# Performance work log

Hardware: AMD Instinct MI355X
Metric: run time of the kernel (lower is better)

## Reference

```python
import jax, jax.numpy as jnp
import numpy as np

NUM_HEADS = 2
POOL_K = 256
REPEAT = 20


def setup_inputs() -> dict:
    key = jax.random.key(0)
    k1, k2, k3 = jax.random.split(key, 3)
    C = 6144
    d = C // NUM_HEADS                      # 3072
    N = REPEAT * (d // POOL_K)              # 240, required by Pq add
    x = jax.random.normal(k1, (N, C), dtype=jnp.float32)
    w_qkv = jax.random.normal(k2, (3 * C, C), dtype=jnp.float32) * 0.02
    w_proj = jax.random.normal(k3, (C, C), dtype=jnp.float32) * 0.02
    b_proj = jnp.zeros((C,), dtype=jnp.float32)
    return {"x": x, "w_qkv": w_qkv, "w_proj": w_proj, "b_proj": b_proj}


def reference(x, w_qkv, w_proj, b_proj):
    N, C = x.shape
    H = NUM_HEADS
    d = C // H
    scale = d ** -0.5
    # qkv: (N, 3C) -> (N, 3, H, d) -> (3, H, N, d)
    qkv = (x @ w_qkv.T).reshape(N, 3, H, d).transpose(1, 2, 0, 3)
    q, k, v = qkv[0], qkv[1], qkv[2]        # each (H, N, d)
    # MaxPool1d(256) over last dim, then tile x20 along last dim -> (H, N, N)
    Pq = q.reshape(H, N, d // POOL_K, POOL_K).max(axis=-1)
    Pq = jnp.tile(Pq, (1, 1, REPEAT))       # (H, N, N)
    attn = jnp.einsum('hnd,hmd->hnm', q, k) * scale + 0.1 * Pq
    attn = jax.nn.softmax(attn, axis=-1)
    out = jnp.einsum('hnm,hmd->hnd', attn, v)    # (H, N, d)
    out = out.transpose(1, 0, 2).reshape(N, C)
    return out @ w_proj.T + b_proj
```

## Files before the change

### kernel.cpp

```cpp
#include <hip/hip_runtime.h>
#include <hip/hip_bf16.h>

#define NN 240
#define CC 6144
#define DD 3072
#define C3 18432
#define HH 2

typedef __attribute__((ext_vector_type(8))) short bf16x8;
typedef __attribute__((ext_vector_type(4))) float f32x4;
typedef unsigned short ushort_t;

static __device__ __forceinline__ unsigned short f2bf(float f) {
    __hip_bfloat16 h = __float2bfloat16(f);
    return __builtin_bit_cast(unsigned short, h);
}

#define GLDS16(g, l) __builtin_amdgcn_global_load_lds( \
    (const __attribute__((address_space(1))) void*)(g), \
    (__attribute__((address_space(3))) void*)(l), 16, 0, 0)

__global__ __launch_bounds__(256, 2)
void gemm_rs(const ushort_t* __restrict__ Ab, int lda, long long sAz,
             const float* __restrict__ B, int ldb, long long sBz,
             const float* __restrict__ bias,
             float* __restrict__ C0, long long sC0z,
             float* __restrict__ CP, long long sCPz,
             int ldc, int N, int Kc, int KS,
             ushort_t* __restrict__ Qb) {
    __shared__ ushort_t sA[2][256 * 64];

    const int zc = blockIdx.z;
    const int z = zc / KS, kc = zc % KS;
    const ushort_t* Abase = Ab + (size_t)z * sAz + (size_t)kc * Kc;
    const float*    Bbase = B  + (size_t)z * sBz + (size_t)kc * Kc;
    float* Cw = (kc == 0) ? (C0 + (size_t)z * sC0z)
                          : (CP + (size_t)(z * (KS - 1) + kc - 1) * sCPz);

    const int n0 = blockIdx.x * 64;
    const int tid = threadIdx.x, lane = tid & 63, wid = tid >> 6;
    const int l16 = lane & 15, lk = lane >> 4;

    const ushort_t* ap = Abase + (size_t)(wid * 64 + (lane >> 3)) * lda
                         + ((lane & 7) ^ ((lane >> 3) & 7)) * 8;

    int colc = n0 + wid * 16 + l16; if (colc > N - 1) colc = N - 1;
    const float* bp = Bbase + (size_t)colc * ldb + lk * 8;

    const int nt = Kc / 64;
    f32x4 acc[16] = {};

    auto ISSUE_A = [&](int u, int par) {
        const ushort_t* a = ap + (size_t)u * 64;
        ushort_t* d = &sA[par][wid * 8 * 512];
#pragma unroll
        for (int i = 0; i < 8; ++i)
            GLDS16(a + (size_t)i * 8 * lda, d + i * 512);
    };
    auto LOAD_B4 = [&](int u, float4& b0, float4& b1, float4& b2, float4& b3) {
        const float* p = bp + (size_t)u * 64;
        b0 = *(const float4*)p;
        b1 = *(const float4*)(p + 4);
        b2 = *(const float4*)(p + 32);
        b3 = *(const float4*)(p + 36);
    };
    auto PHASE = [&](int buf, int ph, float4 g0, float4 g1) {
        bf16x8 bfr;
        bfr[0] = (short)f2bf(g0.x); bfr[1] = (short)f2bf(g0.y);
        bfr[2] = (short)f2bf(g0.z); bfr[3] = (short)f2bf(g0.w);
        bfr[4] = (short)f2bf(g1.x); bfr[5] = (short)f2bf(g1.y);
        bfr[6] = (short)f2bf(g1.z); bfr[7] = (short)f2bf(g1.w);
        const char* As = (const char*)sA[buf];
        __builtin_amdgcn_s_setprio(1);
#pragma unroll
        for (int mt = 0; mt < 16; ++mt) {
            int row = mt * 16 + l16;
            int boff = row * 128 + (((ph * 4 + lk) * 16) ^ ((row & 7) << 4));
            bf16x8 af = *(const bf16x8*)(As + boff);
            acc[mt] = __builtin_amdgcn_mfma_f32_16x16x32_bf16(
                af, bfr, acc[mt], 0, 0, 0);
        }
        __builtin_amdgcn_s_setprio(0);
    };

    float4 e0, e1, e2, e3, o0, o1, o2, o3;

    ISSUE_A(0, 0);
    LOAD_B4(0, e0, e1, e2, e3);
    LOAD_B4(nt > 1 ? 1 : 0, o0, o1, o2, o3);
    __builtin_amdgcn_sched_barrier(0);

    auto STEP = [&](int t,
                    float4& r0, float4& r1, float4& r2, float4& r3,
                    float4& w0, float4& w1, float4& w2, float4& w3) {
        asm volatile("s_waitcnt vmcnt(4)" ::: "memory");
        __builtin_amdgcn_s_barrier();
        __builtin_amdgcn_sched_barrier(0);
        int ua = t + 1 < nt ? t + 1 : nt - 1;
        ISSUE_A(ua, (t + 1) & 1);
        __builtin_amdgcn_sched_barrier(0);
        PHASE(t & 1, 0, r0, r1);
        PHASE(t & 1, 1, r2, r3);
        __builtin_amdgcn_sched_barrier(0);
        int ub = t + 2 < nt ? t + 2 : nt - 1;
        LOAD_B4(ub, w0, w1, w2, w3);
        __builtin_amdgcn_sched_barrier(0);
    };

    for (int t = 0; t < nt; t += 2) {
        STEP(t,     e0, e1, e2, e3, e0, e1, e2, e3);
        STEP(t + 1, o0, o1, o2, o3, o0, o1, o2, o3);
    }

#pragma unroll
    for (int mt = 0; mt < 16; ++mt) {
#pragma unroll
        for (int j = 0; j < 4; ++j) {
            int grow = mt * 16 + lk * 4 + j;
            if (grow < NN) {
                int gcol = n0 + wid * 16 + l16;
                if (gcol < N) {
                    float v = acc[mt][j];
                    if (kc == 0 && bias) v += bias[gcol];
                    Cw[(size_t)grow * ldc + gcol] = v;
                    if (Qb && gcol < CC)
                        Qb[(size_t)grow * CC + gcol] = f2bf(v);
                }
            }
        }
    }
}

__global__ __launch_bounds__(256)
void convert_kernel(const float* __restrict__ x, ushort_t* __restrict__ xb) {
    int id = blockIdx.x * 256 + threadIdx.x;
    int row = id / 768, c8 = id % 768;
    bf16x8 o = {};
    if (row < NN) {
        const float* p = x + (size_t)row * CC + c8 * 8;
        float4 a = *(const float4*)p, b = *(const float4*)(p + 4);
        o[0] = (short)f2bf(a.x); o[1] = (short)f2bf(a.y);
        o[2] = (short)f2bf(a.z); o[3] = (short)f2bf(a.w);
        o[4] = (short)f2bf(b.x); o[5] = (short)f2bf(b.y);
        o[6] = (short)f2bf(b.z); o[7] = (short)f2bf(b.w);
    }
    *(bf16x8*)(xb + (size_t)row * CC + c8 * 8) = o;
}

__global__ __launch_bounds__(256)
void reduce_proj(float4* __restrict__ o4, const float4* __restrict__ p4,
                 long long s4) {
    int i = blockIdx.x * 256 + threadIdx.x;
    float4 a = o4[i];
#pragma unroll
    for (int k = 0; k < 2; ++k) {
        float4 b = p4[(size_t)k * s4 + i];
        a.x += b.x; a.y += b.y; a.z += b.z; a.w += b.w;
    }
    o4[i] = a;
}

__global__ __launch_bounds__(256)
void qmax_kernel(const float* __restrict__ qkv, float* __restrict__ qmax) {
    int idx = blockIdx.x * 4 + (threadIdx.x >> 6);
    int lane = threadIdx.x & 63;
    int c = idx % 12;
    int r = idx / 12;
    int n = r % NN, h = r / NN;
    const float* p = qkv + (size_t)n * C3 + h * DD + c * 256 + lane * 4;
    float4 f = *(const float4*)p;
    float m = fmaxf(fmaxf(f.x, f.y), fmaxf(f.z, f.w));
#pragma unroll
    for (int off = 32; off >= 1; off >>= 1)
        m = fmaxf(m, __shfl_xor(m, off));
    if (lane == 0) qmax[idx] = m;
}

__global__ __launch_bounds__(256)
void softmax_kernel(float* __restrict__ attn, const float* __restrict__ gpart,
                    int ksm1, const float* __restrict__ qmax) {
    int r = blockIdx.x * 4 + (threadIdx.x >> 6);
    int lane = threadIdx.x & 63;
    int z = r / NN, n = r % NN;
    float* row = attn + (size_t)r * NN;
    const float* qm = qmax + r * 12;
    const float scale = 0.0180421959f;
    float v[4];
    float mx = -1e30f;
#pragma unroll
    for (int i = 0; i < 4; ++i) {
        int m = lane + 64 * i;
        v[i] = -1e30f;
        if (m < NN) {
            float s = row[m];
            for (int kc = 0; kc < ksm1; ++kc)
                s += gpart[(size_t)(z * ksm1 + kc) * (NN * NN)
                           + (size_t)n * NN + m];
            v[i] = s * scale + 0.1f * qm[m % 12];
        }
        mx = fmaxf(mx, v[i]);
    }
#pragma unroll
    for (int off = 32; off >= 1; off >>= 1)
        mx = fmaxf(mx, __shfl_xor(mx, off));
    float s = 0.f;
#pragma unroll
    for (int i = 0; i < 4; ++i) {
        v[i] = __expf(v[i] - mx);
        s += v[i];
    }
#pragma unroll
    for (int off = 32; off >= 1; off >>= 1)
        s += __shfl_xor(s, off);
    float inv = 1.0f / s;
#pragma unroll
    for (int i = 0; i < 4; ++i) {
        int m = lane + 64 * i;
        if (m < NN) row[m] = v[i] * inv;
    }
}

__global__ __launch_bounds__(256)
void pv_kernel(const float* __restrict__ attn, const float* __restrict__ qkv,
               ushort_t* __restrict__ preb) {
    const int h = blockIdx.z;
    const int n0 = blockIdx.y * 16;
    const int dd0 = blockIdx.x * 256;
    __shared__ float s_attn[16 * NN];
    for (int i = threadIdx.x; i < 16 * NN; i += 256)
        s_attn[i] = attn[(size_t)h * NN * NN + (n0 + i / NN) * NN + (i % NN)];
    __syncthreads();

    const float* vp = qkv + 2 * CC + h * DD + dd0 + threadIdx.x;
    float acc[16] = {};
    for (int m = 0; m < NN; m += 4) {
        float v0 = vp[(size_t)(m + 0) * C3];
        float v1 = vp[(size_t)(m + 1) * C3];
        float v2 = vp[(size_t)(m + 2) * C3];
        float v3 = vp[(size_t)(m + 3) * C3];
#pragma unroll
        for (int i = 0; i < 16; ++i) {
            float4 a = *(const float4*)&s_attn[i * NN + m];
            acc[i] += a.x * v0 + a.y * v1 + a.z * v2 + a.w * v3;
        }
    }
#pragma unroll
    for (int i = 0; i < 16; ++i)
        preb[(size_t)(n0 + i) * CC + h * DD + dd0 + threadIdx.x] =
            f2bf(acc[i]);
}

extern "C" void kernel_launch(void* const* d_in, const int* in_sizes, int n_in,
                              void* d_out, int out_size, void* d_ws, size_t ws_size,
                              hipStream_t stream) {
    const float* x      = (const float*)d_in[0];
    const float* w_qkv  = (const float*)d_in[1];
    const float* w_proj = (const float*)d_in[2];
    const float* b_proj = (const float*)d_in[3];
    float* out = (float*)d_out;

    const size_t f_qkv  = (size_t)NN * C3;
    const size_t f_attn = (size_t)HH * NN * NN;
    const size_t f_qmax = (size_t)HH * NN * 12;
    float* qkv   = (float*)d_ws;
    float* attn  = qkv + f_qkv;
    float* qmaxb = attn + f_attn;
    ushort_t* xb   = (ushort_t*)(qmaxb + f_qmax);
    ushort_t* qb   = xb + (size_t)256 * CC;
    ushort_t* preb = qb + (size_t)256 * CC;
    float* gpart = (float*)(preb + (size_t)256 * CC);

    convert_kernel<<<768, 256, 0, stream>>>(x, xb);

    gemm_rs<<<dim3(C3 / 64, 1, 1), 256, 0, stream>>>(
        xb, CC, 0LL, w_qkv, CC, 0LL, nullptr,
        qkv, 0LL, gpart, 0LL,
        C3, C3, CC, 1, qb);

    qmax_kernel<<<1440, 256, 0, stream>>>(qkv, qmaxb);

    gemm_rs<<<dim3(4, 1, HH * 24), 256, 0, stream>>>(
        qb, CC, (long long)DD,
        qkv + CC, C3, (long long)DD, nullptr,
        attn, (long long)(NN * NN), gpart, (long long)(NN * NN),
        NN, NN, DD / 24, 24, nullptr);

    softmax_kernel<<<120, 256, 0, stream>>>(attn, gpart, 23, qmaxb);

    pv_kernel<<<dim3(12, 15, HH), 256, 0, stream>>>(attn, qkv, preb);

    gemm_rs<<<dim3(CC / 64, 1, 3), 256, 0, stream>>>(
        preb, CC, 0LL, w_proj, CC, 0LL, b_proj,
        out, 0LL, gpart, (long long)((size_t)NN * CC),
        CC, CC, CC / 3, 3, nullptr);
    reduce_proj<<<1440, 256, 0, stream>>>((float4*)out, (const float4*)gpart,
        (long long)((size_t)NN * CC / 4));
}
```

Before: 404.7 us.

## Pre-convert QKV weights to bf16 and use a bf16×bf16 GEMM kernel

Adds a conversion pass that writes w_qkv (18432×6144 fp32) to a bf16 buffer in the workspace. A new GEMM kernel then reads bf16 B fragments directly into registers, replacing the path that read fp32 weights and converted them inside the GEMM. It runs only when the workspace is large enough, and otherwise falls back to the old kernel. The GEMM now reads half as many weight bytes, but every call pays a full fp32 read plus a bf16 write of the weight matrix in the conversion pass, which may cost more than it saves.

```diff
diff --git a/kernel.cpp b/kernel.cpp
--- a/kernel.cpp
+++ b/kernel.cpp
@@ -131,6 +131,115 @@
     }
 }
 
+__global__ __launch_bounds__(256, 2)
+void gemm_bb(const ushort_t* __restrict__ Ab, int lda,
+             const ushort_t* __restrict__ Bb, int ldb,
+             float* __restrict__ C0, int ldc, int N, int Kc,
+             ushort_t* __restrict__ Qb) {
+    __shared__ ushort_t sA[2][256 * 64];
+
+    const int n0 = blockIdx.x * 64;
+    const int tid = threadIdx.x, lane = tid & 63, wid = tid >> 6;
+    const int l16 = lane & 15, lk = lane >> 4;
+
+    const ushort_t* ap = Ab + (size_t)(wid * 64 + (lane >> 3)) * lda
+                         + ((lane & 7) ^ ((lane >> 3) & 7)) * 8;
+
+    int colc = n0 + wid * 16 + l16; if (colc > N - 1) colc = N - 1;
+    const ushort_t* bp = Bb + (size_t)colc * ldb + lk * 8;
+
+    const int nt = Kc / 64;
+    f32x4 acc[16] = {};
+
+    auto ISSUE_A = [&](int u, int par) {
+        const ushort_t* a = ap + (size_t)u * 64;
+        ushort_t* d = &sA[par][wid * 8 * 512];
+#pragma unroll
+        for (int i = 0; i < 8; ++i)
+            GLDS16(a + (size_t)i * 8 * lda, d + i * 512);
+    };
+    auto LOAD_B2 = [&](int u, bf16x8& b0, bf16x8& b1) {
+        const ushort_t* p = bp + (size_t)u * 64;
+        b0 = *(const bf16x8*)p;
+        b1 = *(const bf16x8*)(p + 32);
+    };
+    auto PHASE = [&](int buf, int ph, bf16x8 bfr) {
+        const char* As = (const char*)sA[buf];
+        __builtin_amdgcn_s_setprio(1);
+#pragma unroll
+        for (int mt = 0; mt < 16; ++mt) {
+            int row = mt * 16 + l16;
+            int boff = row * 128 + (((ph * 4 + lk) * 16) ^ ((row & 7) << 4));
+            bf16x8 af = *(const bf16x8*)(As + boff);
+            acc[mt] = __builtin_amdgcn_mfma_f32_16x16x32_bf16(
+                af, bfr, acc[mt], 0, 0, 0);
+        }
+        __builtin_amdgcn_s_setprio(0);
+    };
+
+    bf16x8 e0, e1, o0, o1;
+
+    ISSUE_A(0, 0);
+    LOAD_B2(0, e0, e1);
+    LOAD_B2(nt > 1 ? 1 : 0, o0, o1);
+    __builtin_amdgcn_sched_barrier(0);
+
+    auto STEP = [&](int t, bf16x8& r0, bf16x8& r1, bf16x8& w0, bf16x8& w1) {
+        asm volatile("s_waitcnt vmcnt(2)" ::: "memory");
+        __builtin_amdgcn_s_barrier();
+        __builtin_amdgcn_sched_barrier(0);
+        int ua = t + 1 < nt ? t + 1 : nt - 1;
+        ISSUE_A(ua, (t + 1) & 1);
+        __builtin_amdgcn_sched_barrier(0);
+        PHASE(t & 1, 0, r0);
+        PHASE(t & 1, 1, r1);
+        __builtin_amdgcn_sched_barrier(0);
+        int ub = t + 2 < nt ? t + 2 : nt - 1;
+        LOAD_B2(ub, w0, w1);
+        __builtin_amdgcn_sched_barrier(0);
+    };
+
+    for (int t = 0; t < nt; t += 2) {
+        STEP(t,     e0, e1, e0, e1);
+        STEP(t + 1, o0, o1, o0, o1);
+    }
+
+#pragma unroll
+    for (int mt = 0; mt < 16; ++mt) {
+#pragma unroll
+        for (int j = 0; j < 4; ++j) {
+            int grow = mt * 16 + lk * 4 + j;
+            if (grow < NN) {
+                int gcol = n0 + wid * 16 + l16;
+                if (gcol < N) {
+                    float v = acc[mt][j];
+                    Cw_store:
+                    C0[(size_t)grow * ldc + gcol] = v;
+                    if (Qb && gcol < CC)
+                        Qb[(size_t)grow * CC + gcol] = f2bf(v);
+                }
+            }
+        }
+    }
+}
+
+__global__ __launch_bounds__(256)
+void conv_w(const float* __restrict__ w, ushort_t* __restrict__ wb,
+            long long n8) {
+    long long i = (long long)blockIdx.x * 256 + threadIdx.x;
+    const long long stride = (long long)gridDim.x * 256;
+    for (; i < n8; i += stride) {
+        const float* p = w + i * 8;
+        float4 a = *(const float4*)p, b = *(const float4*)(p + 4);
+        bf16x8 o;
+        o[0] = (short)f2bf(a.x); o[1] = (short)f2bf(a.y);
+        o[2] = (short)f2bf(a.z); o[3] = (short)f2bf(a.w);
+        o[4] = (short)f2bf(b.x); o[5] = (short)f2bf(b.y);
+        o[6] = (short)f2bf(b.z); o[7] = (short)f2bf(b.w);
+        *(bf16x8*)(wb + i * 8) = o;
+    }
+}
+
 __global__ __launch_bounds__(256)
 void convert_kernel(const float* __restrict__ x, ushort_t* __restrict__ xb) {
     int id = blockIdx.x * 256 + threadIdx.x;
@@ -269,13 +378,26 @@
     ushort_t* qb   = xb + (size_t)256 * CC;
     ushort_t* preb = qb + (size_t)256 * CC;
     float* gpart = (float*)(preb + (size_t)256 * CC);
+    ushort_t* wqb = (ushort_t*)(gpart + f_qkv);
+
+    const size_t base_floats = f_qkv + f_attn + f_qmax
+                             + ((size_t)3 * 256 * CC) / 2 + f_qkv;
+    const size_t need = (base_floats + (size_t)C3 * CC / 2) * 4;
+    const bool big = ws_size >= need;
 
     convert_kernel<<<768, 256, 0, stream>>>(x, xb);
 
-    gemm_rs<<<dim3(C3 / 64, 1, 1), 256, 0, stream>>>(
-        xb, CC, 0LL, w_qkv, CC, 0LL, nullptr,
-        qkv, 0LL, gpart, 0LL,
-        C3, C3, CC, 1, qb);
+    if (big) {
+        conv_w<<<4096, 256, 0, stream>>>(w_qkv, wqb,
+                                         (long long)((size_t)C3 * CC / 8));
+        gemm_bb<<<dim3(C3 / 64, 1, 1), 256, 0, stream>>>(
+            xb, CC, wqb, CC, qkv, C3, C3, CC, qb);
+    } else {
+        gemm_rs<<<dim3(C3 / 64, 1, 1), 256, 0, stream>>>(
+            xb, CC, 0LL, w_qkv, CC, 0LL, nullptr,
+            qkv, 0LL, gpart, 0LL,
+            C3, C3, CC, 1, qb);
+    }
 
     qmax_kernel<<<1440, 256, 0, stream>>>(qkv, qmaxb);
 
```

New measurement: 493.4 us. 21.9% more time.
